# Optimization experiments

Measured on AMD Instinct MI355X. Metric: run time of the kernel, lower is better.

The kernel has to match this reference:

```python
import jax, jax.numpy as jnp
import numpy as np

C = 64            # number of classes (all assumed present in y)
NUM_OVERLAP = 64  # int(args.d * args.overlap_ratio) = int(256 * 0.25)
ALPHA = 1.0       # args.alpha


def setup_inputs() -> dict:
    key = jax.random.key(0)
    k1, k2 = jax.random.split(key)
    x = jax.random.normal(k1, (65536, 512), dtype=jnp.float32)
    y = jax.random.randint(k2, (65536,), 0, C)
    return {"x": x, "y": y}


def reference(x, y):
    # one-hot class membership [C, N]
    member = (y[None, :] == jnp.arange(C)[:, None])
    counts = member.sum(axis=1).astype(x.dtype)                    # [C]
    # class centers: mean of member rows -> [C, D]
    centers = (member.astype(x.dtype) @ x) / counts[:, None]
    # pairwise L2 distance from every center to every sample, [C, N],
    # via ||c||^2 + ||x||^2 - 2 c.x (avoids [C, N, D] intermediate)
    c2 = jnp.sum(centers * centers, axis=1)[:, None]               # [C, 1]
    x2 = jnp.sum(x * x, axis=1)[None, :]                           # [1, N]
    d2 = c2 + x2 - 2.0 * (centers @ x.T)                           # [C, N]
    dist = jnp.sqrt(jnp.maximum(d2, 1e-12))
    neg_inf = jnp.asarray(-jnp.inf, dist.dtype)
    # positives: largest NUM_OVERLAP distances among same-class samples
    pos_vals = jax.lax.top_k(jnp.where(member, dist, neg_inf), NUM_OVERLAP)[0]
    pos_mean = pos_vals.mean(axis=1)                               # [C]
    # negatives: smallest NUM_OVERLAP distances among other-class samples
    neg_vals = -jax.lax.top_k(jnp.where(member, neg_inf, -dist), NUM_OVERLAP)[0]
    neg_mean = neg_vals.mean(axis=1)                               # [C]
    per_class = jnp.maximum(ALPHA + pos_mean - neg_mean, 0.0)
    loss = jnp.sum(per_class) / (C * NUM_OVERLAP)
    return loss.reshape(1)
```

## Files before the change

### kernel.cpp

```cpp
#include <hip/hip_runtime.h>
#include <math.h>

#define N_SAMP 65536
#define DIM    512
#define NCLS   64
#define KSEL   64

#define OFF_COUNTS   0u
#define OFF_CSUM     256u
#define OFF_CENTERS  131328u
#define OFF_C2       196864u
#define OFF_MEANS    197120u
#define OFF_DONE     197632u
#define OFF_DIST     198144u

typedef __attribute__((ext_vector_type(8))) short bf16x8;
typedef __attribute__((ext_vector_type(4))) float f32x4;

__device__ __forceinline__ unsigned short f2bf_rne(float f) {
  const unsigned u = __float_as_uint(f);
  return (unsigned short)((u + 0x7FFFu + ((u >> 16) & 1u)) >> 16);
}

__global__ __launch_bounds__(256) void k_init(int* __restrict__ counts,
                                              float* __restrict__ csum,
                                              unsigned* __restrict__ done) {
  const int i = blockIdx.x * 256 + threadIdx.x;
  const int stride = gridDim.x * 256;
  if (i < NCLS) counts[i] = 0;
  if (i == 0) *done = 0u;
  for (int j = i; j < NCLS * DIM; j += stride) csum[j] = 0.f;
}

__global__ __launch_bounds__(256) void k_class_sums(const float* __restrict__ x,
                                                    const int* __restrict__ y,
                                                    float* __restrict__ csum,
                                                    int* __restrict__ counts) {
  __shared__ int list[4096];
  __shared__ int lcnt;
  const int c  = blockIdx.x >> 4;
  const int r0 = (blockIdx.x & 15) * 4096;
  const int tid = threadIdx.x;
  if (tid == 0) lcnt = 0;
  __syncthreads();
  for (int i = tid; i < 4096; i += 256) {
    if (y[r0 + i] == c) { int p = atomicAdd(&lcnt, 1); list[p] = r0 + i; }
  }
  __syncthreads();
  const int n = lcnt;
  const int dbase = (tid >> 6) * 128 + (tid & 63) * 2;
  float a0 = 0.f, a1 = 0.f, b0 = 0.f, b1 = 0.f;
  int i = 0;
  for (; i + 2 <= n; i += 2) {
    const float* p0 = x + (size_t)list[i] * DIM + dbase;
    const float* p1 = x + (size_t)list[i + 1] * DIM + dbase;
    a0 += p0[0]; a1 += p0[1];
    b0 += p1[0]; b1 += p1[1];
  }
  if (i < n) { const float* p0 = x + (size_t)list[i] * DIM + dbase; a0 += p0[0]; a1 += p0[1]; }
  a0 += b0; a1 += b1;
  atomicAdd(&csum[c * DIM + dbase], a0);
  atomicAdd(&csum[c * DIM + dbase + 1], a1);
  if (tid == 0) atomicAdd(&counts[c], n);
}

__global__ __launch_bounds__(64) void k_centers(const float* __restrict__ csum,
                                                const int* __restrict__ counts,
                                                unsigned short* __restrict__ cenb,
                                                float* __restrict__ c2) {
  const int c = blockIdx.x, l = threadIdx.x;
  const float inv = 1.0f / (float)counts[c];
  float ss = 0.f;
  #pragma unroll
  for (int j = 0; j < 8; ++j) {
    int d = j * 64 + l;
    float v = csum[c * DIM + d] * inv;
    cenb[c * DIM + d] = f2bf_rne(v);
    ss += v * v;
  }
  #pragma unroll
  for (int o = 32; o; o >>= 1) ss += __shfl_down(ss, o, 64);
  if (l == 0) c2[c] = ss;
}

#define CSTR 520
__global__ __launch_bounds__(512, 4) void k_dist_mfma(const float* __restrict__ x,
                                                      const unsigned short* __restrict__ cenb,
                                                      const float* __restrict__ c2,
                                                      float* __restrict__ dist) {
  __shared__ unsigned short cenS[NCLS * CSTR];
  __shared__ float c2s[NCLS];

  const int tid = threadIdx.x;
  const int wave = tid >> 6;
  const int lane = tid & 63;
  const int s0 = blockIdx.x * 128 + wave * 16;
  const int samp = s0 + (lane & 15);
  const int kg = lane >> 4;

  for (int q = tid; q < 4096; q += 512) {
    const int row = q >> 6, cc = q & 63;
    const uint4 v = *reinterpret_cast<const uint4*>(cenb + row * DIM + cc * 8);
    *reinterpret_cast<uint4*>(&cenS[row * CSTR + cc * 8]) = v;
  }
  if (tid < NCLS) c2s[tid] = c2[tid];
  __syncthreads();

  f32x4 acc[4] = {f32x4{0,0,0,0}, f32x4{0,0,0,0}, f32x4{0,0,0,0}, f32x4{0,0,0,0}};
  float x2 = 0.f;
  const float* __restrict__ xrow = x + (size_t)samp * DIM + kg * 8;
  const int arow = lane & 15;

  #pragma unroll 4
  for (int s = 0; s < 16; ++s) {
    const int k0 = s * 32;
    float xf[8];
    *reinterpret_cast<float4*>(&xf[0]) = *reinterpret_cast<const float4*>(xrow + k0);
    *reinterpret_cast<float4*>(&xf[4]) = *reinterpret_cast<const float4*>(xrow + k0 + 4);
    bf16x8 bfrag;
    #pragma unroll
    for (int j = 0; j < 8; ++j) {
      x2 = fmaf(xf[j], xf[j], x2);
      const unsigned u = __float_as_uint(xf[j]);
      bfrag[j] = (short)((u + 0x7FFFu + ((u >> 16) & 1u)) >> 16);
    }
    const int kidx = k0 + kg * 8;
    const bf16x8 a0 = *reinterpret_cast<const bf16x8*>(&cenS[(arow +  0) * CSTR + kidx]);
    const bf16x8 a1 = *reinterpret_cast<const bf16x8*>(&cenS[(arow + 16) * CSTR + kidx]);
    const bf16x8 a2 = *reinterpret_cast<const bf16x8*>(&cenS[(arow + 32) * CSTR + kidx]);
    const bf16x8 a3 = *reinterpret_cast<const bf16x8*>(&cenS[(arow + 48) * CSTR + kidx]);
    acc[0] = __builtin_amdgcn_mfma_f32_16x16x32_bf16(a0, bfrag, acc[0], 0, 0, 0);
    acc[1] = __builtin_amdgcn_mfma_f32_16x16x32_bf16(a1, bfrag, acc[1], 0, 0, 0);
    acc[2] = __builtin_amdgcn_mfma_f32_16x16x32_bf16(a2, bfrag, acc[2], 0, 0, 0);
    acc[3] = __builtin_amdgcn_mfma_f32_16x16x32_bf16(a3, bfrag, acc[3], 0, 0, 0);
  }

  x2 += __shfl_xor(x2, 16, 64);
  x2 += __shfl_xor(x2, 32, 64);

  const int col = s0 + (lane & 15);
  #pragma unroll
  for (int t = 0; t < 4; ++t) {
    #pragma unroll
    for (int r = 0; r < 4; ++r) {
      const int cls = t * 16 + (lane >> 4) * 4 + r;
      const float d2 = c2s[cls] + x2 - 2.0f * acc[t][r];
      dist[(size_t)cls * N_SAMP + col] = sqrtf(fmaxf(d2, 1e-12f));
    }
  }
}

__device__ __forceinline__ void redSix(float v0, float v1, float v2, float v3, float v4, float v5,
                                       float* redf, float* bcast) {
  #pragma unroll
  for (int o = 32; o; o >>= 1) {
    v0 += __shfl_xor(v0, o, 64);
    v1 += __shfl_xor(v1, o, 64);
    v2 = fminf(v2, __shfl_xor(v2, o, 64));
    v3 = fmaxf(v3, __shfl_xor(v3, o, 64));
    v4 += __shfl_xor(v4, o, 64);
    v5 += __shfl_xor(v5, o, 64);
  }
  const int wid = threadIdx.x >> 6;
  if ((threadIdx.x & 63) == 0) {
    redf[wid] = v0; redf[16 + wid] = v1; redf[32 + wid] = v2;
    redf[48 + wid] = v3; redf[64 + wid] = v4; redf[80 + wid] = v5;
  }
  __syncthreads();
  if (threadIdx.x < 16) {
    const int l = threadIdx.x;
    float a0 = redf[l], a1 = redf[16 + l], a2 = redf[32 + l],
          a3 = redf[48 + l], a4 = redf[64 + l], a5 = redf[80 + l];
    #pragma unroll
    for (int o = 8; o; o >>= 1) {
      a0 += __shfl_xor(a0, o, 64);
      a1 += __shfl_xor(a1, o, 64);
      a2 = fminf(a2, __shfl_xor(a2, o, 64));
      a3 = fmaxf(a3, __shfl_xor(a3, o, 64));
      a4 += __shfl_xor(a4, o, 64);
      a5 += __shfl_xor(a5, o, 64);
    }
    if (l == 0) { bcast[0]=a0; bcast[1]=a1; bcast[2]=a2; bcast[3]=a3; bcast[4]=a4; bcast[5]=a5; }
  }
  __syncthreads();
}

__global__ __launch_bounds__(1024, 4) void k_select2(const float* __restrict__ dist,
                                                     const int* __restrict__ y,
                                                     float* __restrict__ means,
                                                     unsigned* __restrict__ done,
                                                     float* __restrict__ out) {
  __shared__ unsigned bitmap[2048];
  __shared__ unsigned hist[1024];
  __shared__ unsigned wscan[16];
  __shared__ float redf[96];
  __shared__ float bcast[8];
  __shared__ float bbuf[1024];
  __shared__ int bcnt_s;
  __shared__ int bsel;
  __shared__ int lastflag;

  const int tid = threadIdx.x;
  const int c = blockIdx.x >> 1;
  const int neg = blockIdx.x & 1;
  const float* __restrict__ row = dist + (size_t)c * N_SAMP;

  if (tid == 0) { bcnt_s = 0; bsel = 1023; lastflag = 0; }

  #pragma unroll
  for (int j = 0; j < 2; ++j) {
    unsigned wbits = 0u;
    const int base = tid * 64 + j * 32;
    #pragma unroll
    for (int b = 0; b < 32; ++b) wbits |= (unsigned)(y[base + b] == c) << b;
    bitmap[tid * 2 + j] = wbits;
  }
  __syncthreads();

  const float qnan = __uint_as_float(0x7fc00000u);
  float vals[64];
  float mn = 1e30f, mx = -1e30f;
  #pragma unroll
  for (int i = 0; i < 64; ++i) {
    const int n = i * 1024 + tid;
    const unsigned bit = (bitmap[n >> 5] >> (n & 31)) & 1u;
    float v = row[n];
    if (!neg) v = -v;
    const float vv = ((int)bit != neg) ? v : qnan;
    vals[i] = vv;
    mn = fminf(mn, vv);
    mx = fmaxf(mx, vv);
  }
  redSix(0.f, 0.f, mn, mx, 0.f, 0.f, redf, bcast);
  const float lo = bcast[2], hi = bcast[3];

  float meanval;
  if (!(hi > lo)) {
    meanval = neg ? lo : -lo;
  } else {
    const float scale = 1024.0f / (hi - lo);
    hist[tid] = 0u;
    __syncthreads();
    #pragma unroll
    for (int i = 0; i < 64; ++i) {
      const float v = vals[i];
      if (v >= lo && v <= hi) {
        int b = (int)((v - lo) * scale);
        b = b < 1023 ? b : 1023; b = b > 0 ? b : 0;
        atomicAdd(&hist[b], 1u);
      }
    }
    __syncthreads();
    const int lane = tid & 63, wid = tid >> 6;
    const unsigned h = hist[tid];
    unsigned cum = h;
    #pragma unroll
    for (int d = 1; d < 64; d <<= 1) {
      const unsigned t = (unsigned)__shfl_up((int)cum, d, 64);
      if (lane >= d) cum += t;
    }
    if (lane == 63) wscan[wid] = cum;
    __syncthreads();
    if (tid < 16) {
      unsigned v = wscan[tid];
      #pragma unroll
      for (int d = 1; d < 16; d <<= 1) {
        const unsigned t = (unsigned)__shfl_up((int)v, d, 64);
        if (tid >= d) v += t;
      }
      wscan[tid] = v;
    }
    __syncthreads();
    const unsigned full = cum + (wid ? wscan[wid - 1] : 0u);
    hist[tid] = full;
    const unsigned prev = full - h;
    if (full >= (unsigned)KSEL && prev < (unsigned)KSEL) bsel = tid;
    __syncthreads();
    const int B = bsel;
    const unsigned SC = B ? hist[B - 1] : 0u;
    const int need = KSEL - (int)SC;

    float ss = 0.f;
    #pragma unroll
    for (int i = 0; i < 64; ++i) {
      const float v = vals[i];
      if (v >= lo && v <= hi) {
        int b = (int)((v - lo) * scale);
        b = b < 1023 ? b : 1023; b = b > 0 ? b : 0;
        if (b < B) ss += v;
        else if (b == B) {
          const int p = atomicAdd(&bcnt_s, 1);
          if (p < 1024) bbuf[p] = v;
        }
      }
    }
    redSix(ss, 0.f, 0.f, 0.f, 0.f, 0.f, redf, bcast);
    const float SS = bcast[0];
    const int cnt = bcnt_s;
    float bsum = 0.f;

    if (cnt <= 1024) {
      const int L = (cnt <= 256) ? 256 : 1024;
      if (tid < L) bbuf[tid] = (tid < cnt) ? bbuf[tid] : __uint_as_float(0x7F800000u);
      __syncthreads();
      for (int k = 2; k <= L; k <<= 1) {
        for (int j = k >> 1; j > 0; j >>= 1) {
          const int ixj = tid ^ j;
          float a = 0.f, b2 = 0.f;
          if (tid < L) { a = bbuf[tid]; b2 = bbuf[ixj]; }
          __syncthreads();
          if (tid < L && ixj > tid) {
            const bool asc = ((tid & k) == 0);
            if ((a > b2) == asc) { bbuf[tid] = b2; bbuf[ixj] = a; }
          }
          __syncthreads();
        }
      }
      float v = (tid < need) ? bbuf[tid] : 0.f;
      redSix(v, 0.f, 0.f, 0.f, 0.f, 0.f, redf, bcast);
      bsum = bcast[0];
    } else {
      float thr = -1e30f;
      int rem2 = need;
      for (int g = 0; g < 64 && rem2 > 0; ++g) {
        float m = 1e30f;
        #pragma unroll
        for (int i = 0; i < 64; ++i) {
          const float v = vals[i];
          if (v >= lo && v <= hi) {
            int b = (int)((v - lo) * scale);
            b = b < 1023 ? b : 1023; b = b > 0 ? b : 0;
            if (b == B && v > thr) m = fminf(m, v);
          }
        }
        redSix(0.f, 0.f, m, 0.f, 0.f, 0.f, redf, bcast);
        const float M = bcast[2];
        float ce = 0.f;
        #pragma unroll
        for (int i = 0; i < 64; ++i) {
          const float v = vals[i];
          if (v >= lo && v <= hi) {
            int b = (int)((v - lo) * scale);
            b = b < 1023 ? b : 1023; b = b > 0 ? b : 0;
            if (b == B && v == M) ce += 1.f;
          }
        }
        redSix(0.f, 0.f, 0.f, 0.f, ce, 0.f, redf, bcast);
        const int CE = (int)bcast[4];
        const int take = rem2 < CE ? rem2 : CE;
        bsum += (float)take * M;
        rem2 -= take;
        thr = M;
      }
    }
    const float total = SS + bsum;
    meanval = neg ? total * (1.0f / 64.0f) : -total * (1.0f / 64.0f);
  }

  if (tid == 0) {
    __hip_atomic_store(&means[neg * 64 + c], meanval, __ATOMIC_RELAXED, __HIP_MEMORY_SCOPE_AGENT);
    const unsigned old = __hip_atomic_fetch_add(done, 1u, __ATOMIC_ACQ_REL, __HIP_MEMORY_SCOPE_AGENT);
    lastflag = (old == 127u) ? 1 : 0;
  }
  __syncthreads();
  if (lastflag && tid < 64) {
    const float pm = __hip_atomic_load(&means[tid], __ATOMIC_ACQUIRE, __HIP_MEMORY_SCOPE_AGENT);
    const float nm = __hip_atomic_load(&means[64 + tid], __ATOMIC_ACQUIRE, __HIP_MEMORY_SCOPE_AGENT);
    float pc = fmaxf(1.0f + pm - nm, 0.0f);
    #pragma unroll
    for (int o = 32; o; o >>= 1) pc += __shfl_down(pc, o, 64);
    if (tid == 0) out[0] = pc * (1.0f / 4096.0f);
  }
}

extern "C" void kernel_launch(void* const* d_in, const int* in_sizes, int n_in,
                              void* d_out, int out_size, void* d_ws, size_t ws_size,
                              hipStream_t stream) {
  const float* x = (const float*)d_in[0];
  const int* y = (const int*)d_in[1];
  float* out = (float*)d_out;
  char* w = (char*)d_ws;
  int* counts          = (int*)(w + OFF_COUNTS);
  float* csum          = (float*)(w + OFF_CSUM);
  unsigned short* cenb = (unsigned short*)(w + OFF_CENTERS);
  float* c2            = (float*)(w + OFF_C2);
  float* means         = (float*)(w + OFF_MEANS);
  unsigned* done       = (unsigned*)(w + OFF_DONE);
  float* dist          = (float*)(w + OFF_DIST);

  hipLaunchKernelGGL(k_init, dim3(64), dim3(256), 0, stream, counts, csum, done);
  hipLaunchKernelGGL(k_class_sums, dim3(1024), dim3(256), 0, stream, x, y, csum, counts);
  hipLaunchKernelGGL(k_centers, dim3(64), dim3(64), 0, stream, csum, counts, cenb, c2);
  hipLaunchKernelGGL(k_dist_mfma, dim3(N_SAMP / 128), dim3(512), 0, stream, x, cenb, c2, dist);
  hipLaunchKernelGGL(k_select2, dim3(128), dim3(1024), 0, stream, dist, y, means, done, out);
}
```

Before: 101.8 us.

## Emit bf16 copy of x during class sums and merge pos/neg selection per block

The class-sum kernel now also writes a bf16 copy of x, so the distance kernel reads half the bytes and computes x^2 from the bf16 values. When the workspace is too small it falls back to the f32 distance kernel. The selection kernel handles both positive and negative top-k for a class in one block, reading each distance row once. It uses a 4096-bin histogram with a block scan, and one wave peels the boundary bin instead of doing a block-wide bitonic sort. Risks: the extra bf16 write traffic, x^2 now computed from rounded values, and only 64 selection blocks, which gives less parallelism.

Result: slower. 210.8 us (+107.0%).

```diff
diff --git a/kernel.cpp b/kernel.cpp
--- a/kernel.cpp
+++ b/kernel.cpp
@@ -5,6 +5,7 @@
 #define DIM    512
 #define NCLS   64
 #define KSEL   64
+#define SNBIN  4096
 
 #define OFF_COUNTS   0u
 #define OFF_CSUM     256u
@@ -12,7 +13,10 @@
 #define OFF_C2       196864u
 #define OFF_MEANS    197120u
 #define OFF_DONE     197632u
-#define OFF_DIST     198144u
+#define OFF_XB       262144u
+#define OFF_DIST     67371008u
+#define WS_NEED      84148224u
+#define OFF_DIST_FB  262144u
 
 typedef __attribute__((ext_vector_type(8))) short bf16x8;
 typedef __attribute__((ext_vector_type(4))) float f32x4;
@@ -35,7 +39,8 @@
 __global__ __launch_bounds__(256) void k_class_sums(const float* __restrict__ x,
                                                     const int* __restrict__ y,
                                                     float* __restrict__ csum,
-                                                    int* __restrict__ counts) {
+                                                    int* __restrict__ counts,
+                                                    unsigned* __restrict__ xb32) {
   __shared__ int list[4096];
   __shared__ int lcnt;
   const int c  = blockIdx.x >> 4;
@@ -49,15 +54,28 @@
   __syncthreads();
   const int n = lcnt;
   const int dbase = (tid >> 6) * 128 + (tid & 63) * 2;
+  const int xoff = dbase >> 1;
   float a0 = 0.f, a1 = 0.f, b0 = 0.f, b1 = 0.f;
   int i = 0;
   for (; i + 2 <= n; i += 2) {
-    const float* p0 = x + (size_t)list[i] * DIM + dbase;
-    const float* p1 = x + (size_t)list[i + 1] * DIM + dbase;
-    a0 += p0[0]; a1 += p0[1];
-    b0 += p1[0]; b1 += p1[1];
-  }
-  if (i < n) { const float* p0 = x + (size_t)list[i] * DIM + dbase; a0 += p0[0]; a1 += p0[1]; }
+    const int r0i = list[i], r1i = list[i + 1];
+    const float* p0 = x + (size_t)r0i * DIM + dbase;
+    const float* p1 = x + (size_t)r1i * DIM + dbase;
+    const float v00 = p0[0], v01 = p0[1], v10 = p1[0], v11 = p1[1];
+    a0 += v00; a1 += v01;
+    b0 += v10; b1 += v11;
+    if (xb32) {
+      xb32[(size_t)r0i * 256 + xoff] = (unsigned)f2bf_rne(v00) | ((unsigned)f2bf_rne(v01) << 16);
+      xb32[(size_t)r1i * 256 + xoff] = (unsigned)f2bf_rne(v10) | ((unsigned)f2bf_rne(v11) << 16);
+    }
+  }
+  if (i < n) {
+    const int ri = list[i];
+    const float* p0 = x + (size_t)ri * DIM + dbase;
+    const float v00 = p0[0], v01 = p0[1];
+    a0 += v00; a1 += v01;
+    if (xb32) xb32[(size_t)ri * 256 + xoff] = (unsigned)f2bf_rne(v00) | ((unsigned)f2bf_rne(v01) << 16);
+  }
   a0 += b0; a1 += b1;
   atomicAdd(&csum[c * DIM + dbase], a0);
   atomicAdd(&csum[c * DIM + dbase + 1], a1);
@@ -84,10 +102,10 @@
 }
 
 #define CSTR 520
-__global__ __launch_bounds__(512, 4) void k_dist_mfma(const float* __restrict__ x,
-                                                      const unsigned short* __restrict__ cenb,
-                                                      const float* __restrict__ c2,
-                                                      float* __restrict__ dist) {
+__global__ __launch_bounds__(512, 4) void k_dist_bf(const unsigned short* __restrict__ xb,
+                                                    const unsigned short* __restrict__ cenb,
+                                                    const float* __restrict__ c2,
+                                                    float* __restrict__ dist) {
   __shared__ unsigned short cenS[NCLS * CSTR];
   __shared__ float c2s[NCLS];
 
@@ -108,21 +126,23 @@
 
   f32x4 acc[4] = {f32x4{0,0,0,0}, f32x4{0,0,0,0}, f32x4{0,0,0,0}, f32x4{0,0,0,0}};
   float x2 = 0.f;
-  const float* __restrict__ xrow = x + (size_t)samp * DIM + kg * 8;
+  const unsigned short* __restrict__ xrow = xb + (size_t)samp * DIM + kg * 8;
   const int arow = lane & 15;
 
   #pragma unroll 4
   for (int s = 0; s < 16; ++s) {
     const int k0 = s * 32;
-    float xf[8];
-    *reinterpret_cast<float4*>(&xf[0]) = *reinterpret_cast<const float4*>(xrow + k0);
-    *reinterpret_cast<float4*>(&xf[4]) = *reinterpret_cast<const float4*>(xrow + k0 + 4);
-    bf16x8 bfrag;
-    #pragma unroll
-    for (int j = 0; j < 8; ++j) {
-      x2 = fmaf(xf[j], xf[j], x2);
-      const unsigned u = __float_as_uint(xf[j]);
-      bfrag[j] = (short)((u + 0x7FFFu + ((u >> 16) & 1u)) >> 16);
+    const bf16x8 bfrag = *reinterpret_cast<const bf16x8*>(xrow + k0);
+    const uint4 bu = *reinterpret_cast<const uint4*>(&bfrag);
+    {
+      const unsigned dw[4] = {bu.x, bu.y, bu.z, bu.w};
+      #pragma unroll
+      for (int q = 0; q < 4; ++q) {
+        const float flo = __uint_as_float(dw[q] << 16);
+        const float fhi = __uint_as_float(dw[q] & 0xFFFF0000u);
+        x2 = fmaf(flo, flo, x2);
+        x2 = fmaf(fhi, fhi, x2);
+      }
     }
     const int kidx = k0 + kg * 8;
     const bf16x8 a0 = *reinterpret_cast<const bf16x8*>(&cenS[(arow +  0) * CSTR + kidx]);
@@ -150,16 +170,76 @@
   }
 }
 
-__device__ __forceinline__ void redSix(float v0, float v1, float v2, float v3, float v4, float v5,
-                                       float* redf, float* bcast) {
+__global__ __launch_bounds__(512, 4) void k_dist_f32(const float* __restrict__ x,
+                                                     const unsigned short* __restrict__ cenb,
+                                                     const float* __restrict__ c2,
+                                                     float* __restrict__ dist) {
+  __shared__ unsigned short cenS[NCLS * CSTR];
+  __shared__ float c2s[NCLS];
+  const int tid = threadIdx.x;
+  const int wave = tid >> 6;
+  const int lane = tid & 63;
+  const int s0 = blockIdx.x * 128 + wave * 16;
+  const int samp = s0 + (lane & 15);
+  const int kg = lane >> 4;
+  for (int q = tid; q < 4096; q += 512) {
+    const int row = q >> 6, cc = q & 63;
+    const uint4 v = *reinterpret_cast<const uint4*>(cenb + row * DIM + cc * 8);
+    *reinterpret_cast<uint4*>(&cenS[row * CSTR + cc * 8]) = v;
+  }
+  if (tid < NCLS) c2s[tid] = c2[tid];
+  __syncthreads();
+  f32x4 acc[4] = {f32x4{0,0,0,0}, f32x4{0,0,0,0}, f32x4{0,0,0,0}, f32x4{0,0,0,0}};
+  float x2 = 0.f;
+  const float* __restrict__ xrow = x + (size_t)samp * DIM + kg * 8;
+  const int arow = lane & 15;
+  #pragma unroll 4
+  for (int s = 0; s < 16; ++s) {
+    const int k0 = s * 32;
+    float xf[8];
+    *reinterpret_cast<float4*>(&xf[0]) = *reinterpret_cast<const float4*>(xrow + k0);
+    *reinterpret_cast<float4*>(&xf[4]) = *reinterpret_cast<const float4*>(xrow + k0 + 4);
+    bf16x8 bfrag;
+    #pragma unroll
+    for (int j = 0; j < 8; ++j) {
+      x2 = fmaf(xf[j], xf[j], x2);
+      const unsigned u = __float_as_uint(xf[j]);
+      bfrag[j] = (short)((u + 0x7FFFu + ((u >> 16) & 1u)) >> 16);
+    }
+    const int kidx = k0 + kg * 8;
+    const bf16x8 a0 = *reinterpret_cast<const bf16x8*>(&cenS[(arow +  0) * CSTR + kidx]);
+    const bf16x8 a1 = *reinterpret_cast<const bf16x8*>(&cenS[(arow + 16) * CSTR + kidx]);
+    const bf16x8 a2 = *reinterpret_cast<const bf16x8*>(&cenS[(arow + 32) * CSTR + kidx]);
+    const bf16x8 a3 = *reinterpret_cast<const bf16x8*>(&cenS[(arow + 48) * CSTR + kidx]);
+    acc[0] = __builtin_amdgcn_mfma_f32_16x16x32_bf16(a0, bfrag, acc[0], 0, 0, 0);
+    acc[1] = __builtin_amdgcn_mfma_f32_16x16x32_bf16(a1, bfrag, acc[1], 0, 0, 0);
+    acc[2] = __builtin_amdgcn_mfma_f32_16x16x32_bf16(a2, bfrag, acc[2], 0, 0, 0);
+    acc[3] = __builtin_amdgcn_mfma_f32_16x16x32_bf16(a3, bfrag, acc[3], 0, 0, 0);
+  }
+  x2 += __shfl_xor(x2, 16, 64);
+  x2 += __shfl_xor(x2, 32, 64);
+  const int col = s0 + (lane & 15);
+  #pragma unroll
+  for (int t = 0; t < 4; ++t) {
+    #pragma unroll
+    for (int r = 0; r < 4; ++r) {
+      const int cls = t * 16 + (lane >> 4) * 4 + r;
+      const float d2 = c2s[cls] + x2 - 2.0f * acc[t][r];
+      dist[(size_t)cls * N_SAMP + col] = sqrtf(fmaxf(d2, 1e-12f));
+    }
+  }
+}
+
+__device__ __forceinline__ void redSix2(float v0, float v1, float v2, float v3, float v4, float v5,
+                                        float* redf, float* bcast) {
   #pragma unroll
   for (int o = 32; o; o >>= 1) {
     v0 += __shfl_xor(v0, o, 64);
     v1 += __shfl_xor(v1, o, 64);
     v2 = fminf(v2, __shfl_xor(v2, o, 64));
     v3 = fmaxf(v3, __shfl_xor(v3, o, 64));
-    v4 += __shfl_xor(v4, o, 64);
-    v5 += __shfl_xor(v5, o, 64);
+    v4 = fminf(v4, __shfl_xor(v4, o, 64));
+    v5 = fmaxf(v5, __shfl_xor(v5, o, 64));
   }
   const int wid = threadIdx.x >> 6;
   if ((threadIdx.x & 63) == 0) {
@@ -177,36 +257,111 @@
       a1 += __shfl_xor(a1, o, 64);
       a2 = fminf(a2, __shfl_xor(a2, o, 64));
       a3 = fmaxf(a3, __shfl_xor(a3, o, 64));
-      a4 += __shfl_xor(a4, o, 64);
-      a5 += __shfl_xor(a5, o, 64);
+      a4 = fminf(a4, __shfl_xor(a4, o, 64));
+      a5 = fmaxf(a5, __shfl_xor(a5, o, 64));
     }
     if (l == 0) { bcast[0]=a0; bcast[1]=a1; bcast[2]=a2; bcast[3]=a3; bcast[4]=a4; bcast[5]=a5; }
   }
   __syncthreads();
 }
 
-__global__ __launch_bounds__(1024, 4) void k_select2(const float* __restrict__ dist,
+__device__ __forceinline__ int binS(float w, float lo, float sc) {
+  int b = (int)((w - lo) * sc);
+  b = b < SNBIN - 1 ? b : SNBIN - 1;
+  return b > 0 ? b : 0;
+}
+
+__device__ __forceinline__ void scanFind(const unsigned* hseg, int K, unsigned* wscan,
+                                         int* bsel, unsigned* strict) {
+  const int tid = threadIdx.x;
+  const int lane = tid & 63, wid = tid >> 6;
+  unsigned b4[4]; unsigned s4 = 0;
+  #pragma unroll
+  for (int j = 0; j < 4; ++j) { b4[j] = hseg[tid * 4 + j]; s4 += b4[j]; }
+  unsigned cum = s4;
+  #pragma unroll
+  for (int d = 1; d < 64; d <<= 1) {
+    const unsigned t = (unsigned)__shfl_up((int)cum, d, 64);
+    if (lane >= d) cum += t;
+  }
+  if (lane == 63) wscan[wid] = cum;
+  __syncthreads();
+  if (tid < 16) {
+    unsigned v = wscan[tid];
+    #pragma unroll
+    for (int d = 1; d < 16; d <<= 1) {
+      const unsigned t = (unsigned)__shfl_up((int)v, d, 64);
+      if (tid >= d) v += t;
+    }
+    wscan[tid] = v;
+  }
+  __syncthreads();
+  const unsigned gcum = cum + (wid ? wscan[wid - 1] : 0u);
+  const unsigned gprev = gcum - s4;
+  if (gcum >= (unsigned)K && gprev < (unsigned)K) {
+    unsigned run = gprev;
+    #pragma unroll
+    for (int j = 0; j < 4; ++j) {
+      if (run + b4[j] >= (unsigned)K) { *bsel = tid * 4 + j; *strict = run; break; }
+      run += b4[j];
+    }
+  }
+  __syncthreads();
+}
+
+__device__ __forceinline__ float wavePeel(const float* buf, int cnt, int need, int lane) {
+  float thr = -1e30f, s = 0.f;
+  int taken = 0;
+  for (int g = 0; g < 64 && taken < need; ++g) {
+    float m = 1e30f;
+    for (int t = 0; t < 16; ++t) {
+      const int idx = lane + t * 64;
+      if (idx < cnt) { const float u = buf[idx]; if (u > thr) m = fminf(m, u); }
+    }
+    #pragma unroll
+    for (int o = 32; o; o >>= 1) m = fminf(m, __shfl_xor(m, o, 64));
+    int ce = 0;
+    for (int t = 0; t < 16; ++t) {
+      const int idx = lane + t * 64;
+      if (idx < cnt && buf[idx] == m) ++ce;
+    }
+    #pragma unroll
+    for (int o = 32; o; o >>= 1) ce += __shfl_xor(ce, o, 64);
+    const int take = (need - taken) < ce ? (need - taken) : ce;
+    s += (float)take * m;
+    taken += take;
+    thr = m;
+  }
+  return s;
+}
+
+__global__ __launch_bounds__(1024, 4) void k_select3(const float* __restrict__ dist,
                                                      const int* __restrict__ y,
                                                      float* __restrict__ means,
                                                      unsigned* __restrict__ done,
                                                      float* __restrict__ out) {
   __shared__ unsigned bitmap[2048];
-  __shared__ unsigned hist[1024];
+  __shared__ unsigned hist[2 * SNBIN];
   __shared__ unsigned wscan[16];
   __shared__ float redf[96];
   __shared__ float bcast[8];
-  __shared__ float bbuf[1024];
-  __shared__ int bcnt_s;
-  __shared__ int bsel;
+  __shared__ float bbufP[1024];
+  __shared__ float bbufN[1024];
+  __shared__ int cntP, cntN, bselP, bselN;
+  __shared__ unsigned strictP, strictN;
+  __shared__ float bsumP, bsumN;
   __shared__ int lastflag;
 
   const int tid = threadIdx.x;
-  const int c = blockIdx.x >> 1;
-  const int neg = blockIdx.x & 1;
+  const int lane = tid & 63;
+  const int wid = tid >> 6;
+  const int c = blockIdx.x;
   const float* __restrict__ row = dist + (size_t)c * N_SAMP;
 
-  if (tid == 0) { bcnt_s = 0; bsel = 1023; lastflag = 0; }
-
+  if (tid == 0) {
+    cntP = 0; cntN = 0; bselP = 0; bselN = 0;
+    strictP = 0u; strictN = 0u; bsumP = 0.f; bsumN = 0.f; lastflag = 0;
+  }
   #pragma unroll
   for (int j = 0; j < 2; ++j) {
     unsigned wbits = 0u;
@@ -217,150 +372,128 @@
   }
   __syncthreads();
 
-  const float qnan = __uint_as_float(0x7fc00000u);
   float vals[64];
-  float mn = 1e30f, mx = -1e30f;
+  unsigned long long mb = 0ull;
+  float mnP = 1e30f, mxP = -1e30f, mnN = 1e30f, mxN = -1e30f;
+  #pragma unroll
+  for (int i = 0; i < 16; ++i) {
+    const int base = i * 4096 + tid * 4;
+    const float4 v4 = *reinterpret_cast<const float4*>(row + base);
+    const unsigned bits = bitmap[base >> 5] >> (base & 31);
+    const float vv[4] = {v4.x, v4.y, v4.z, v4.w};
+    #pragma unroll
+    for (int j = 0; j < 4; ++j) {
+      const unsigned bit = (bits >> j) & 1u;
+      const float v = vv[j];
+      vals[i * 4 + j] = v;
+      mb |= (unsigned long long)bit << (i * 4 + j);
+      if (bit) { const float w = -v; mnP = fminf(mnP, w); mxP = fmaxf(mxP, w); }
+      else     { mnN = fminf(mnN, v); mxN = fmaxf(mxN, v); }
+    }
+  }
+  redSix2(0.f, 0.f, mnP, mxP, mnN, mxN, redf, bcast);
+  const float loP = bcast[2], hiP = bcast[3], loN = bcast[4], hiN = bcast[5];
+  const bool degP = !(hiP > loP), degN = !(hiN > loN);
+  const float scP = degP ? 0.f : (float)SNBIN / (hiP - loP);
+  const float scN = degN ? 0.f : (float)SNBIN / (hiN - loN);
+
+  for (int i = tid; i < 2 * SNBIN; i += 1024) hist[i] = 0u;
+  __syncthreads();
+
   #pragma unroll
   for (int i = 0; i < 64; ++i) {
-    const int n = i * 1024 + tid;
-    const unsigned bit = (bitmap[n >> 5] >> (n & 31)) & 1u;
-    float v = row[n];
-    if (!neg) v = -v;
-    const float vv = ((int)bit != neg) ? v : qnan;
-    vals[i] = vv;
-    mn = fminf(mn, vv);
-    mx = fmaxf(mx, vv);
-  }
-  redSix(0.f, 0.f, mn, mx, 0.f, 0.f, redf, bcast);
-  const float lo = bcast[2], hi = bcast[3];
-
-  float meanval;
-  if (!(hi > lo)) {
-    meanval = neg ? lo : -lo;
-  } else {
-    const float scale = 1024.0f / (hi - lo);
-    hist[tid] = 0u;
-    __syncthreads();
-    #pragma unroll
-    for (int i = 0; i < 64; ++i) {
-      const float v = vals[i];
-      if (v >= lo && v <= hi) {
-        int b = (int)((v - lo) * scale);
-        b = b < 1023 ? b : 1023; b = b > 0 ? b : 0;
-        atomicAdd(&hist[b], 1u);
+    const float v = vals[i];
+    if ((mb >> i) & 1ull) { if (!degP) atomicAdd(&hist[binS(-v, loP, scP)], 1u); }
+    else                  { if (!degN) atomicAdd(&hist[SNBIN + binS(v, loN, scN)], 1u); }
+  }
+  __syncthreads();
+
+  scanFind(&hist[0],     KSEL, wscan, &bselP, &strictP);
+  scanFind(&hist[SNBIN], KSEL, wscan, &bselN, &strictN);
+  const int BP = bselP, BN = bselN;
+
+  float ssP = 0.f, ssN = 0.f;
+  #pragma unroll
+  for (int i = 0; i < 64; ++i) {
+    const float v = vals[i];
+    if ((mb >> i) & 1ull) {
+      if (!degP) {
+        const int b = binS(-v, loP, scP);
+        if (b < BP) ssP += -v;
+        else if (b == BP) { const int p = atomicAdd(&cntP, 1); if (p < 1024) bbufP[p] = -v; }
       }
-    }
-    __syncthreads();
-    const int lane = tid & 63, wid = tid >> 6;
-    const unsigned h = hist[tid];
-    unsigned cum = h;
-    #pragma unroll
-    for (int d = 1; d < 64; d <<= 1) {
-      const unsigned t = (unsigned)__shfl_up((int)cum, d, 64);
-      if (lane >= d) cum += t;
-    }
-    if (lane == 63) wscan[wid] = cum;
-    __syncthreads();
-    if (tid < 16) {
-      unsigned v = wscan[tid];
+    } else {
+      if (!degN) {
+        const int b = binS(v, loN, scN);
+        if (b < BN) ssN += v;
+        else if (b == BN) { const int p = atomicAdd(&cntN, 1); if (p < 1024) bbufN[p] = v; }
+      }
+    }
+  }
+  redSix2(ssP, ssN, 0.f, 0.f, 0.f, 0.f, redf, bcast);
+  const float SSP = bcast[0], SSN = bcast[1];
+  const int CP = cntP, CN = cntN;
+  const int needP = KSEL - (int)strictP, needN = KSEL - (int)strictN;
+
+  if (wid == 0 && !degP && CP <= 1024) {
+    const float s = wavePeel(bbufP, CP, needP, lane);
+    if (lane == 0) bsumP = s;
+  }
+  if (wid == 1 && !degN && CN <= 1024) {
+    const float s = wavePeel(bbufN, CN, needN, lane);
+    if (lane == 0) bsumN = s;
+  }
+  __syncthreads();
+
+  for (int role = 0; role < 2; ++role) {
+    const bool deg = role ? degN : degP;
+    const int cnt = role ? CN : CP;
+    if (deg || cnt <= 1024) continue;
+    const int B = role ? BN : BP;
+    const int need = role ? needN : needP;
+    const float lo = role ? loN : loP, sc = role ? scN : scP;
+    float thr = -1e30f, accum = 0.f;
+    int taken = 0;
+    for (int g = 0; g < 64 && taken < need; ++g) {
+      float m = 1e30f;
       #pragma unroll
-      for (int d = 1; d < 16; d <<= 1) {
-        const unsigned t = (unsigned)__shfl_up((int)v, d, 64);
-        if (tid >= d) v += t;
-      }
-      wscan[tid] = v;
-    }
-    __syncthreads();
-    const unsigned full = cum + (wid ? wscan[wid - 1] : 0u);
-    hist[tid] = full;
-    const unsigned prev = full - h;
-    if (full >= (unsigned)KSEL && prev < (unsigned)KSEL) bsel = tid;
-    __syncthreads();
-    const int B = bsel;
-    const unsigned SC = B ? hist[B - 1] : 0u;
-    const int need = KSEL - (int)SC;
-
-    float ss = 0.f;
-    #pragma unroll
-    for (int i = 0; i < 64; ++i) {
-      const float v = vals[i];
-      if (v >= lo && v <= hi) {
-        int b = (int)((v - lo) * scale);
-        b = b < 1023 ? b : 1023; b = b > 0 ? b : 0;
-        if (b < B) ss += v;
-        else if (b == B) {
-          const int p = atomicAdd(&bcnt_s, 1);
-          if (p < 1024) bbuf[p] = v;
+      for (int i = 0; i < 64; ++i) {
+        const int member = (int)((mb >> i) & 1ull);
+        if (member == (role ? 0 : 1)) {
+          const float w = role ? vals[i] : -vals[i];
+          if (binS(w, lo, sc) == B && w > thr) m = fminf(m, w);
         }
       }
-    }
-    redSix(ss, 0.f, 0.f, 0.f, 0.f, 0.f, redf, bcast);
-    const float SS = bcast[0];
-    const int cnt = bcnt_s;
-    float bsum = 0.f;
-
-    if (cnt <= 1024) {
-      const int L = (cnt <= 256) ? 256 : 1024;
-      if (tid < L) bbuf[tid] = (tid < cnt) ? bbuf[tid] : __uint_as_float(0x7F800000u);
-      __syncthreads();
-      for (int k = 2; k <= L; k <<= 1) {
-        for (int j = k >> 1; j > 0; j >>= 1) {
-          const int ixj = tid ^ j;
-          float a = 0.f, b2 = 0.f;
-          if (tid < L) { a = bbuf[tid]; b2 = bbuf[ixj]; }
-          __syncthreads();
-          if (tid < L && ixj > tid) {
-            const bool asc = ((tid & k) == 0);
-            if ((a > b2) == asc) { bbuf[tid] = b2; bbuf[ixj] = a; }
-          }
-          __syncthreads();
+      redSix2(0.f, 0.f, m, 0.f, 0.f, 0.f, redf, bcast);
+      const float M = bcast[2];
+      float ce = 0.f;
+      #pragma unroll
+      for (int i = 0; i < 64; ++i) {
+        const int member = (int)((mb >> i) & 1ull);
+        if (member == (role ? 0 : 1)) {
+          const float w = role ? vals[i] : -vals[i];
+          if (w == M) ce += 1.f;
         }
       }
-      float v = (tid < need) ? bbuf[tid] : 0.f;
-      redSix(v, 0.f, 0.f, 0.f, 0.f, 0.f, redf, bcast);
-      bsum = bcast[0];
-    } else {
-      float thr = -1e30f;
-      int rem2 = need;
-      for (int g = 0; g < 64 && rem2 > 0; ++g) {
-        float m = 1e30f;
-        #pragma unroll
-        for (int i = 0; i < 64; ++i) {
-          const float v = vals[i];
-          if (v >= lo && v <= hi) {
-            int b = (int)((v - lo) * scale);
-            b = b < 1023 ? b : 1023; b = b > 0 ? b : 0;
-            if (b == B && v > thr) m = fminf(m, v);
-          }
-        }
-        redSix(0.f, 0.f, m, 0.f, 0.f, 0.f, redf, bcast);
-        const float M = bcast[2];
-        float ce = 0.f;
-        #pragma unroll
-        for (int i = 0; i < 64; ++i) {
-          const float v = vals[i];
-          if (v >= lo && v <= hi) {
-            int b = (int)((v - lo) * scale);
-            b = b < 1023 ? b : 1023; b = b > 0 ? b : 0;
-            if (b == B && v == M) ce += 1.f;
-          }
-        }
-        redSix(0.f, 0.f, 0.f, 0.f, ce, 0.f, redf, bcast);
-        const int CE = (int)bcast[4];
-        const int take = rem2 < CE ? rem2 : CE;
-        bsum += (float)take * M;
-        rem2 -= take;
-        thr = M;
-      }
-    }
-    const float total = SS + bsum;
-    meanval = neg ? total * (1.0f / 64.0f) : -total * (1.0f / 64.0f);
-  }
+      redSix2(ce, 0.f, 0.f, 0.f, 0.f, 0.f, redf, bcast);
+      const int CE = (int)bcast[0];
+      const int take = (need - taken) < CE ? (need - taken) : CE;
+      accum += (float)take * M;
+      taken += take;
+      thr = M;
+    }
+    if (tid == 0) { if (role) bsumN = accum; else bsumP = accum; }
+    __syncthreads();
+  }
+
+  const float mP = degP ? (-loP) : -(SSP + bsumP) * (1.0f / 64.0f);
+  const float mN = degN ? ( loN) :  (SSN + bsumN) * (1.0f / 64.0f);
 
   if (tid == 0) {
-    __hip_atomic_store(&means[neg * 64 + c], meanval, __ATOMIC_RELAXED, __HIP_MEMORY_SCOPE_AGENT);
+    __hip_atomic_store(&means[c],      mP, __ATOMIC_RELAXED, __HIP_MEMORY_SCOPE_AGENT);
+    __hip_atomic_store(&means[64 + c], mN, __ATOMIC_RELAXED, __HIP_MEMORY_SCOPE_AGENT);
     const unsigned old = __hip_atomic_fetch_add(done, 1u, __ATOMIC_ACQ_REL, __HIP_MEMORY_SCOPE_AGENT);
-    lastflag = (old == 127u) ? 1 : 0;
+    lastflag = (old == (unsigned)(NCLS - 1)) ? 1 : 0;
   }
   __syncthreads();
   if (lastflag && tid < 64) {
@@ -386,11 +519,19 @@
   float* c2            = (float*)(w + OFF_C2);
   float* means         = (float*)(w + OFF_MEANS);
   unsigned* done       = (unsigned*)(w + OFF_DONE);
-  float* dist          = (float*)(w + OFF_DIST);
+
+  const bool big = (ws_size >= (size_t)WS_NEED);
+  float* dist = (float*)(w + (big ? OFF_DIST : OFF_DIST_FB));
+  unsigned* xb32 = big ? (unsigned*)(w + OFF_XB) : (unsigned*)nullptr;
 
   hipLaunchKernelGGL(k_init, dim3(64), dim3(256), 0, stream, counts, csum, done);
-  hipLaunchKernelGGL(k_class_sums, dim3(1024), dim3(256), 0, stream, x, y, csum, counts);
+  hipLaunchKernelGGL(k_class_sums, dim3(1024), dim3(256), 0, stream, x, y, csum, counts, xb32);
   hipLaunchKernelGGL(k_centers, dim3(64), dim3(64), 0, stream, csum, counts, cenb, c2);
-  hipLaunchKernelGGL(k_dist_mfma, dim3(N_SAMP / 128), dim3(512), 0, stream, x, cenb, c2, dist);
-  hipLaunchKernelGGL(k_select2, dim3(128), dim3(1024), 0, stream, dist, y, means, done, out);
-}
+  if (big) {
+    hipLaunchKernelGGL(k_dist_bf, dim3(N_SAMP / 128), dim3(512), 0, stream,
+                       (const unsigned short*)xb32, cenb, c2, dist);
+  } else {
+    hipLaunchKernelGGL(k_dist_f32, dim3(N_SAMP / 128), dim3(512), 0, stream, x, cenb, c2, dist);
+  }
+  hipLaunchKernelGGL(k_select3, dim3(NCLS), dim3(1024), 0, stream, dist, y, means, done, out);
+}
```
